# Kernel optimization log

Hardware: AMD Instinct MI355X
Metric: run time of the kernel (lower is better)

Reference implementation:

```python
import jax, jax.numpy as jnp
import numpy as np

B, S, T = 32, 512, 50          # batch, max seq, topic memory tokens
D, H, F, NL = 512, 8, 2048, 4  # bert-small dims
VB, VOC = 30000, 30522         # bow vocab (VAE), bert vocab


def _ln(x, g, b, eps=1e-12):
    m = x.mean(-1, keepdims=True)
    v = ((x - m) ** 2).mean(-1, keepdims=True)
    return (x - m) * jax.lax.rsqrt(v + eps) * g + b


def setup_inputs() -> dict:
    key = jax.random.key(0)
    ks = iter(jax.random.split(key, 40))
    n = lambda shape, s=0.02: jax.random.normal(next(ks), shape, jnp.float32) * s
    inp = {
        'input_ids': jax.random.randint(next(ks), (B, S), 0, VOC, jnp.int32),
        'seq_lens': jax.random.randint(next(ks), (B,), 1, S + 1, jnp.int32),
        'embed': n((VOC, D)),
        'W_dec': n((T, VB)), 'b_dec': jnp.zeros((VB,), jnp.float32),
        'mem_W1': n((VB, 2 * D)), 'mem_b1': jnp.zeros((2 * D,), jnp.float32),
        'mem_W2': n((2 * D, D)), 'mem_b2': jnp.zeros((D,), jnp.float32),
        'mem_ln_g': jnp.ones((D,), jnp.float32), 'mem_ln_b': jnp.zeros((D,), jnp.float32),
        'Wq': n((NL, D, D)), 'bq': jnp.zeros((NL, D), jnp.float32),
        'Wk': n((NL, D, D)), 'bk': jnp.zeros((NL, D), jnp.float32),
        'Wv': n((NL, D, D)), 'bv': jnp.zeros((NL, D), jnp.float32),
        'Wo': n((NL, D, D)), 'bo': jnp.zeros((NL, D), jnp.float32),
        'ln1_g': jnp.ones((NL, D), jnp.float32), 'ln1_b': jnp.zeros((NL, D), jnp.float32),
        'Wi': n((NL, D, F)), 'bi': jnp.zeros((NL, F), jnp.float32),
        'Wf': n((NL, F, D)), 'bf': jnp.zeros((NL, D), jnp.float32),
        'ln2_g': jnp.ones((NL, D), jnp.float32), 'ln2_b': jnp.zeros((NL, D), jnp.float32),
    }
    return inp


def reference(input_ids, seq_lens, embed, W_dec, b_dec, mem_W1, mem_b1, mem_W2, mem_b2,
              mem_ln_g, mem_ln_b, Wq, bq, Wk, bk, Wv, bv, Wo, bo, ln1_g, ln1_b,
              Wi, bi, Wf, bf, ln2_g, ln2_b):
    # --- topic memory: VAE.decode(eye(T)) == rows of decoder weight ---
    word_dist = jax.nn.softmax(W_dec + b_dec, axis=1)            # [T, VB]
    hmem = jax.nn.relu(word_dist @ mem_W1 + mem_b1)
    topic_memory = _ln(hmem @ mem_W2 + mem_b2, mem_ln_g, mem_ln_b)  # [T, D]

    hidden = embed[input_ids]                                     # [B, S, D]

    # --- vectorized ragged insertion: [real tokens | memory | padding] ---
    lens = jnp.clip(seq_lens, 1, S)[:, None]                      # [B, 1]
    j = jnp.arange(S + T)[None, :]                                # [1, S+T]
    from_mem = (j >= lens) & (j < lens + T)                       # [B, S+T]
    src = jnp.clip(jnp.where(j < lens, j, j - T), 0, S - 1)       # [B, S+T]
    gathered = jnp.take_along_axis(hidden, src[..., None], axis=1)
    mem_idx = jnp.clip(j - lens, 0, T - 1)                        # [B, S+T]
    hidden = jnp.where(from_mem[..., None], topic_memory[mem_idx], gathered)  # [B, S+T, D]
    mask = (j < lens + T).astype(hidden.dtype)                    # [B, S+T]
    bias = (mask - 1.0)[:, None, None, :] * 10000.0               # extended attention mask

    dh = D // H
    scale = 1.0 / np.sqrt(dh)
    for l in range(NL):
        q = (hidden @ Wq[l] + bq[l]).reshape(B, S + T, H, dh)
        k = (hidden @ Wk[l] + bk[l]).reshape(B, S + T, H, dh)
        v = (hidden @ Wv[l] + bv[l]).reshape(B, S + T, H, dh)
        scores = jnp.einsum('bqhd,bkhd->bhqk', q, k) * scale + bias
        attn = jax.nn.softmax(scores, axis=-1)
        ctx = jnp.einsum('bhqk,bkhd->bqhd', attn, v).reshape(B, S + T, D)
        hidden = _ln(hidden + ctx @ Wo[l] + bo[l], ln1_g[l], ln1_b[l])
        ff = jax.nn.gelu(hidden @ Wi[l] + bi[l], approximate=False)
        hidden = _ln(hidden + ff @ Wf[l] + bf[l], ln2_g[l], ln2_b[l])
    return hidden
```

## Files before the change

kernel.cpp:

```cpp
#include <hip/hip_runtime.h>
#include <hip/hip_bf16.h>
#include <math.h>

using bf16 = __hip_bfloat16;
typedef __attribute__((ext_vector_type(4))) float f32x4;
typedef __attribute__((ext_vector_type(8))) short short8;

#define B_N 32
#define S_N 512
#define T_N 50
#define H_N 8
#define NL_N 4
#define VB_N 30000
#define VBP_N 30016
#define ST_N 562
#define STP_N 576
#define NTOK_N (B_N*ST_N)
#define WCH_N 16
#define WCW_N 1875

__device__ __forceinline__ float b2f(bf16 x){ return __bfloat162float(x); }
__device__ __forceinline__ bf16  f2b(float x){ return __float2bfloat16(x); }
__device__ __forceinline__ float ldw(const void* p, long i, int f){
    return f ? ((const float*)p)[i] : __bfloat162float(((const bf16*)p)[i]);
}

__device__ __forceinline__ float gelu_f(float x){
    float z = fabsf(x) * 0.70710678118654752f;
    float t = __builtin_amdgcn_rcpf(__builtin_fmaf(0.3275911f, z, 1.f));
    float p = t*(0.254829592f + t*(-0.284496736f + t*(1.421413741f + t*(-1.453152027f + t*1.061405429f))));
    float er = 1.f - p*__expf(-z*z);
    return 0.5f*x*(1.f + copysignf(er, x));
}

__device__ __forceinline__ void load_lds16(const void* g, void* l){
    __builtin_amdgcn_global_load_lds((const __attribute__((address_space(1))) void*)g,
                                     (__attribute__((address_space(3))) void*)l, 16, 0, 0);
}

__device__ __forceinline__ int xcd_swizzle(int flat, int nwg){
    int xcd = flat & 7, rest = flat >> 3;
    int q = nwg >> 3, r = nwg & 7;
    return (xcd < r ? xcd*(q+1) : r*(q+1) + (xcd-r)*q) + rest;
}

__device__ __forceinline__ float block_reduce_max(float v, float* red, int t){
    for (int o=32;o>0;o>>=1) v = fmaxf(v, __shfl_down(v,o,64));
    int w=t>>6, lane=t&63;
    if (lane==0) red[w]=v;
    __syncthreads();
    return fmaxf(fmaxf(red[0],red[1]),fmaxf(red[2],red[3]));
}
__device__ __forceinline__ float block_reduce_sum(float v, float* red, int t){
    for (int o=32;o>0;o>>=1) v += __shfl_down(v,o,64);
    int w=t>>6, lane=t&63;
    if (lane==0) red[w]=v;
    __syncthreads();
    return red[0]+red[1]+red[2]+red[3];
}

__global__ __launch_bounds__(256) void detect_k(const unsigned int* __restrict__ w, int* flag)
{
    int t = threadIdx.x;
    float s = 0.f;
    for (int i=t;i<4096;i+=256){ int e = (w[i]>>7)&0xFF; s += fabsf((float)e - 120.f); }
    __shared__ float red[4];
    for (int o=32;o>0;o>>=1) s += __shfl_down(s,o,64);
    int wv=t>>6, lane=t&63;
    if (lane==0) red[wv]=s;
    __syncthreads();
    if (t==0) flag[0] = ((red[0]+red[1]+red[2]+red[3]) * (1.f/4096.f) > 20.f) ? 1 : 0;
}

__global__ void zero_u32_k(unsigned int* p, long n){
    long i = (long)blockIdx.x*256 + threadIdx.x;
    if (i < n) p[i] = 0u;
}

__global__ __launch_bounds__(256) void wd_partmax_k(
    const void* __restrict__ Wd, const void* __restrict__ bd,
    float* __restrict__ pmax, const int* __restrict__ flagp)
{
    const int isf = *flagp;
    int ch = blockIdx.x, r = blockIdx.y, t = threadIdx.x;
    int c0 = ch*WCW_N, c1 = c0 + WCW_N;
    __shared__ float red[4];
    float mx = -1e30f;
    for (int c=c0+t;c<c1;c+=256) mx = fmaxf(mx, ldw(Wd,(long)r*VB_N+c,isf) + ldw(bd,c,isf));
    mx = block_reduce_max(mx, red, t);
    if (t==0) pmax[r*WCH_N + ch] = mx;
}

__global__ __launch_bounds__(256) void wd_partsum_k(
    const void* __restrict__ Wd, const void* __restrict__ bd,
    const float* __restrict__ pmax, float* __restrict__ psum, const int* __restrict__ flagp)
{
    const int isf = *flagp;
    int ch = blockIdx.x, r = blockIdx.y, t = threadIdx.x;
    float mx = -1e30f;
    #pragma unroll
    for (int i=0;i<WCH_N;i++) mx = fmaxf(mx, pmax[r*WCH_N+i]);
    int c0 = ch*WCW_N, c1 = c0 + WCW_N;
    __shared__ float red[4];
    float sm = 0.f;
    for (int c=c0+t;c<c1;c+=256) sm += __expf(ldw(Wd,(long)r*VB_N+c,isf) + ldw(bd,c,isf) - mx);
    sm = block_reduce_sum(sm, red, t);
    if (t==0) psum[r*WCH_N + ch] = sm;
}

__global__ __launch_bounds__(256) void wd_write_k(
    const void* __restrict__ Wd, const void* __restrict__ bd,
    const float* __restrict__ pmax, const float* __restrict__ psum,
    bf16* __restrict__ wdb, const int* __restrict__ flagp)
{
    const int isf = *flagp;
    int ch = blockIdx.x, r = blockIdx.y, t = threadIdx.x;
    float mx = -1e30f, sm = 0.f;
    #pragma unroll
    for (int i=0;i<WCH_N;i++){ mx = fmaxf(mx, pmax[r*WCH_N+i]); sm += psum[r*WCH_N+i]; }
    float inv = 1.f/sm;
    int c0 = ch*WCW_N, c1 = c0 + WCW_N;
    for (int c=c0+t;c<c1;c+=256)
        wdb[(long)r*VBP_N + c] = f2b(__expf(ldw(Wd,(long)r*VB_N+c,isf) + ldw(bd,c,isf) - mx)*inv);
}

__global__ __launch_bounds__(256) void relu_bias_k(
    const float* __restrict__ hmem, const void* __restrict__ b1,
    bf16* __restrict__ hrel, const int* __restrict__ flagp)
{
    const int isf = *flagp;
    int r = blockIdx.x, t = threadIdx.x;
    for (int c=t;c<1024;c+=256){
        float v = (r < T_N) ? fmaxf(hmem[r*1024+c] + ldw(b1,c,isf), 0.f) : 0.f;
        hrel[r*1024+c] = f2b(v);
    }
}

__global__ __launch_bounds__(256) void ln_topic_k(
    const float* __restrict__ fcout,
    const void* __restrict__ lg, const void* __restrict__ lb,
    float* __restrict__ tmf, bf16* __restrict__ tmb, const int* __restrict__ flagp)
{
    const int isf = *flagp;
    int r = blockIdx.x, t = threadIdx.x;
    float a0 = fcout[r*512+t], a1 = fcout[r*512+t+256];
    __shared__ float red[4];
    float mean = block_reduce_sum(a0+a1, red, t) * (1.f/512.f);
    float d0=a0-mean, d1=a1-mean;
    __syncthreads();
    float var = block_reduce_sum(d0*d0+d1*d1, red, t) * (1.f/512.f);
    float rstd = rsqrtf(var + 1e-12f);
    float o0 = d0*rstd*ldw(lg,t,isf) + ldw(lb,t,isf);
    float o1 = d1*rstd*ldw(lg,t+256,isf) + ldw(lb,t+256,isf);
    tmf[r*512+t]=o0; tmf[r*512+t+256]=o1;
    tmb[r*512+t]=f2b(o0); tmb[r*512+t+256]=f2b(o1);
}

__global__ __launch_bounds__(256) void embed_insert_k(
    const int* __restrict__ ids, const int* __restrict__ lens,
    const void* __restrict__ embed, const float* __restrict__ tmf,
    const bf16* __restrict__ tmb, float* __restrict__ hf, bf16* __restrict__ hb,
    const int* __restrict__ flagp)
{
    const int isf = *flagp;
    int j = blockIdx.x, b = blockIdx.y, t = threadIdx.x;
    int L = lens[b]; L = L<1?1:(L>S_N?S_N:L);
    long orow = ((long)b*ST_N + j)*512;
    if (j >= L && j < L + T_N) {
        int m = j - L;
        for (int c=t;c<512;c+=256){ float v = tmf[m*512+c]; hf[orow+c]=v; hb[orow+c]=tmb[m*512+c]; }
    } else {
        int sj = (j < L) ? j : j - T_N;
        int id = ids[b*S_N + sj];
        for (int c=t;c<512;c+=256){ float e = ldw(embed,(long)id*512+c,isf); hf[orow+c]=e; hb[orow+c]=f2b(e); }
    }
}

__global__ __launch_bounds__(256) void transpose_k(
    const void* __restrict__ src, bf16* __restrict__ dst,
    int R, int C, long sstride, long dstride, int Ksrc, const int* __restrict__ flagp)
{
    const int isf = *flagp;
    __shared__ bf16 tile[32][33];
    int n0 = blockIdx.x * 32, k0 = blockIdx.y * 32, z = blockIdx.z;
    int t = threadIdx.x;
    int nl = t & 31, kb = t >> 5;
    #pragma unroll
    for (int i=0;i<4;i++) {
        int k = k0 + kb + i*8; k = k < Ksrc ? k : Ksrc-1;
        tile[kb+i*8][nl] = f2b(ldw(src, z*sstride + (long)k*C + n0+nl, isf));
    }
    __syncthreads();
    int kl = t & 31, nb = t >> 5;
    #pragma unroll
    for (int i=0;i<4;i++) {
        int n = nb + i*8;
        dst[z*dstride + (long)(n0+n)*R + k0+kl] = tile[kl][n];
    }
}

__global__ void concat_bias_k(const void* bq, const void* bk, const void* bv, bf16* out,
                              const int* __restrict__ flagp){
    const int isf = *flagp;
    int i = blockIdx.x*256 + threadIdx.x;
    if (i >= NL_N*1536) return;
    int l = i/1536, n = i%1536;
    float v = (n<512) ? ldw(bq,l*512+n,isf) : (n<1024 ? ldw(bk,l*512+n-512,isf) : ldw(bv,l*512+n-1024,isf));
    out[i] = f2b(v);
}

__global__ __launch_bounds__(256) void transpose_v_k(
    const bf16* __restrict__ qkv, bf16* __restrict__ Vt, const int* __restrict__ slens)
{
    __shared__ bf16 tl[64*33];
    int k0 = blockIdx.x * 32, z = blockIdx.z;
    int b = z >> 3, h = z & 7;
    int L = slens[b]; L = L<1?1:(L>S_N?S_N:L);
    int kmax = ((L + T_N + 63) >> 6) << 6;
    if (k0 >= kmax) return;
    int t = threadIdx.x;
    int n = t & 63, kb = t >> 6;
    #pragma unroll
    for (int i=0;i<8;i++) {
        int kl = kb + 4*i;
        int kg = k0 + kl;
        bf16 v = (kg < ST_N) ? qkv[((long)(b*ST_N + kg))*1536 + 1024 + h*64 + n] : f2b(0.f);
        tl[n*33 + kl] = v;
    }
    __syncthreads();
    int kk = t & 31, nb = t >> 5;
    #pragma unroll
    for (int i=0;i<8;i++) {
        int nn = nb + 8*i;
        Vt[((long)z*64 + nn)*STP_N + k0 + kk] = tl[nn*33 + kk];
    }
}

constexpr int EPI_BF16=0, EPI_F32=1, EPI_GELU=2, EPI_ATOMIC=3, EPI_BF16R=4;

template<int BM, int BN, int MODE>
__global__ __launch_bounds__(256,4) void gemm_k(
    const bf16* __restrict__ Ag, const bf16* __restrict__ Bg, void* __restrict__ Cg,
    const void* __restrict__ bias, long bias_off,
    int M, int N, int K, int lda, int ldb, int ldc, int Nst, int kch,
    const int* __restrict__ flagp)
{
    const int isf = *flagp;
    __shared__ __align__(16) bf16 lA[BM*64];
    __shared__ __align__(16) bf16 lB[BN*64];
    const int tid = threadIdx.x;
    const int nwg = gridDim.x * gridDim.y;
    const int flat = blockIdx.y * gridDim.x + blockIdx.x;
    const int swz = xcd_swizzle(flat, nwg);
    const int tile_m = (swz / gridDim.x) * BM;
    const int tile_n = (swz % gridDim.x) * BN;

    bf16*  C16 = (bf16*)Cg;
    float* C32 = (float*)Cg;

    constexpr int WM = BM/2, WN = BN/2, MI = WM/16, NI = WN/16;
    const int w = tid>>6, lane = tid&63;
    const int wm = w>>1, wn = w&1;
    const int quad = lane>>4, lrow = lane&15;

    f32x4 zero = {0.f,0.f,0.f,0.f};
    f32x4 acc[MI][NI];
    #pragma unroll
    for (int i=0;i<MI;i++)
        #pragma unroll
        for (int j=0;j<NI;j++) acc[i][j] = zero;

    int ks = 0, ke = K;
    if (kch > 0) { ks = blockIdx.z * kch; ke = ks + kch; if (ke > K) ke = K; }

    for (int k0=ks;k0<ke;k0+=64) {
        __syncthreads();
        #pragma unroll
        for (int r=0;r<BM/32;r++) {
            int e = r*256 + tid;
            int row = e>>3, c8 = (e&7) ^ (row&7);
            int gr = tile_m + row; gr = gr < M ? gr : M-1;
            load_lds16(Ag + (long)gr*lda + k0 + c8*8, &lA[e*8]);
        }
        #pragma unroll
        for (int r=0;r<BN/32;r++) {
            int e = r*256 + tid;
            int row = e>>3, c8 = (e&7) ^ (row&7);
            int gr = tile_n + row; gr = gr < N ? gr : N-1;
            load_lds16(Bg + (long)gr*ldb + k0 + c8*8, &lB[e*8]);
        }
        __syncthreads();
        #pragma unroll
        for (int kc=0;kc<2;kc++){
            short8 afr[MI], bfr[NI];
            #pragma unroll
            for (int i=0;i<MI;i++){
                int row = wm*WM + i*16 + lrow;
                afr[i] = *(const short8*)&lA[row*64 + (((kc*4+quad) ^ (row&7))<<3)];
            }
            #pragma unroll
            for (int j=0;j<NI;j++){
                int row = wn*WN + j*16 + lrow;
                bfr[j] = *(const short8*)&lB[row*64 + (((kc*4+quad) ^ (row&7))<<3)];
            }
            #pragma unroll
            for (int i=0;i<MI;i++)
                #pragma unroll
                for (int j=0;j<NI;j++)
                    acc[i][j] = __builtin_amdgcn_mfma_f32_16x16x32_bf16(afr[i], bfr[j], acc[i][j], 0, 0, 0);
        }
    }

    float bcol[NI];
    #pragma unroll
    for (int j=0;j<NI;j++){
        int col = tile_n + wn*WN + j*16 + lrow;
        if constexpr (MODE == EPI_ATOMIC) { bcol[j] = 0.f; }
        else if constexpr (MODE == EPI_BF16) {
            bcol[j] = (col < Nst) ? b2f(((const bf16*)bias)[bias_off + col]) : 0.f;
        } else {
            bcol[j] = (col < Nst) ? ldw(bias, bias_off + col, isf) : 0.f;
        }
    }

    #pragma unroll
    for (int i=0;i<MI;i++) {
        #pragma unroll
        for (int j=0;j<NI;j++) {
            int col = tile_n + wn*WN + j*16 + lrow;
            if (col >= Nst) continue;
            int rb  = tile_m + wm*WM + i*16 + quad*4;
            #pragma unroll
            for (int r=0;r<4;r++) {
                int row = rb + r;
                if (row >= M) continue;
                float v = acc[i][j][r];
                if constexpr (MODE == EPI_BF16 || MODE == EPI_BF16R) {
                    C16[(long)row*ldc + col] = f2b(v + bcol[j]);
                } else if constexpr (MODE == EPI_F32) {
                    C32[(long)row*ldc + col] = v + bcol[j];
                } else if constexpr (MODE == EPI_GELU) {
                    C16[(long)row*ldc + col] = f2b(gelu_f(v + bcol[j]));
                } else {
                    atomicAdd(&C32[(long)row*ldc + col], v);
                }
            }
        }
    }
}

__global__ __launch_bounds__(256,3) void flash_k(
    const bf16* __restrict__ qkv, const bf16* __restrict__ Vt,
    bf16* __restrict__ ctx, const int* __restrict__ slens)
{
    __shared__ __align__(16) bf16 lQ[64*64];
    __shared__ __align__(16) bf16 lK[2][64*64];
    __shared__ __align__(16) bf16 lV[2][64*64];
    __shared__ __align__(16) bf16 lP[64*64];
    const int nwg = gridDim.x * gridDim.z;
    const int flat = blockIdx.z * gridDim.x + blockIdx.x;
    const int swz = xcd_swizzle(flat, nwg);
    const int z = swz / gridDim.x, b = z>>3, h = z&7;
    const int qt = swz % gridDim.x;
    const int tid = threadIdx.x;
    const int w = tid>>6, lane = tid&63;
    const int quad = lane>>4, l15 = lane&15;
    int L = slens[b]; L = L<1?1:(L>S_N?S_N:L);
    const int lenT = L + T_N;
    const int nkt = (lenT + 63) >> 6;

    #pragma unroll
    for (int rr=0;rr<2;rr++){
        int ci = rr*256 + tid;
        int row = ci>>3, c8 = (ci&7) ^ (row&7);
        int gr = qt*64 + row; gr = gr < ST_N ? gr : ST_N-1;
        load_lds16(qkv + ((long)(b*ST_N+gr))*1536 + h*64 + c8*8, &lQ[ci*8]);
    }

    auto stage_K = [&](int buf, int kt){
        #pragma unroll
        for (int rr=0;rr<2;rr++){
            int ci = rr*256+tid;
            int row = ci>>3, c8 = (ci&7) ^ (row&7);
            int kr = kt*64+row; kr = kr < ST_N ? kr : ST_N-1;
            load_lds16(qkv + ((long)(b*ST_N+kr))*1536 + 512 + h*64 + c8*8, &lK[buf][ci*8]);
        }
    };
    auto stage_V = [&](int buf, int kt){
        #pragma unroll
        for (int rr=0;rr<2;rr++){
            int ci = rr*256+tid;
            int n = ci>>3, c8 = (ci&7) ^ (n&7);
            load_lds16(Vt + ((long)z*64+n)*STP_N + kt*64 + c8*8, &lV[buf][ci*8]);
        }
    };

    stage_K(0, 0);
    stage_V(0, 0);

    f32x4 zerov = {0.f,0.f,0.f,0.f};
    f32x4 O[4];
    float m_i[4], l_i[4];
    #pragma unroll
    for (int j=0;j<4;j++) O[j] = zerov;
    #pragma unroll
    for (int r=0;r<4;r++){ m_i[r]=-1e30f; l_i[r]=0.f; }

    const int qrow = w*16;

    for (int kt=0; kt<nkt; kt++){
        const int cur = kt & 1;
        __syncthreads();
        if (kt+1 < nkt) stage_K(cur^1, kt+1);

        f32x4 S[4];
        #pragma unroll
        for (int j=0;j<4;j++) S[j] = zerov;
        #pragma unroll
        for (int kc=0;kc<2;kc++){
            short8 aQ, bK[4];
            {
                int row = qrow + l15;
                aQ = *(const short8*)&lQ[row*64 + (((kc*4+quad) ^ (row&7))<<3)];
            }
            #pragma unroll
            for (int j=0;j<4;j++){
                int row = j*16+l15;
                bK[j] = *(const short8*)&lK[cur][row*64 + (((kc*4+quad) ^ (row&7))<<3)];
            }
            #pragma unroll
            for (int j=0;j<4;j++)
                S[j] = __builtin_amdgcn_mfma_f32_16x16x32_bf16(aQ, bK[j], S[j], 0,0,0);
        }

        #pragma unroll
        for (int r=0;r<4;r++){
            float mx = -1e30f;
            #pragma unroll
            for (int j=0;j<4;j++){
                int col = kt*64 + j*16 + l15;
                float s = S[j][r]*0.125f + (col < lenT ? 0.f : -10000.f);
                S[j][r] = s;
                mx = fmaxf(mx, s);
            }
            #pragma unroll
            for (int o=1;o<16;o<<=1) mx = fmaxf(mx, __shfl_xor(mx, o, 64));
            float mn = fmaxf(m_i[r], mx);
            float alpha = __expf(m_i[r] - mn);
            m_i[r] = mn;
            float sm = 0.f;
            #pragma unroll
            for (int j=0;j<4;j++){
                float pv = __expf(S[j][r] - mn);
                S[j][r] = pv;
                sm += pv;
            }
            #pragma unroll
            for (int o=1;o<16;o<<=1) sm += __shfl_xor(sm, o, 64);
            l_i[r] = l_i[r]*alpha + sm;
            #pragma unroll
            for (int j=0;j<4;j++) O[j][r] *= alpha;
        }

        #pragma unroll
        for (int j=0;j<4;j++)
            #pragma unroll
            for (int r=0;r<4;r++){
                int row = qrow + quad*4 + r;
                int col = j*16 + l15;
                lP[row*64 + (((col>>3) ^ (row&7))<<3) + (col&7)] = f2b(S[j][r]);
            }
        __syncthreads();
        if (kt+1 < nkt) stage_V(cur^1, kt+1);

        #pragma unroll
        for (int kc=0;kc<2;kc++){
            short8 aP, bV[4];
            {
                int row = qrow + l15;
                aP = *(const short8*)&lP[row*64 + (((kc*4+quad) ^ (row&7))<<3)];
            }
            #pragma unroll
            for (int j=0;j<4;j++){
                int row = j*16+l15;
                bV[j] = *(const short8*)&lV[cur][row*64 + (((kc*4+quad) ^ (row&7))<<3)];
            }
            #pragma unroll
            for (int j=0;j<4;j++)
                O[j] = __builtin_amdgcn_mfma_f32_16x16x32_bf16(aP, bV[j], O[j], 0,0,0);
        }
    }

    #pragma unroll
    for (int r=0;r<4;r++){
        int row = qt*64 + qrow + quad*4 + r;
        if (row >= ST_N) continue;
        float inv_l = __builtin_amdgcn_rcpf(l_i[r]);
        #pragma unroll
        for (int j=0;j<4;j++)
            ctx[((long)(b*ST_N+row))*512 + h*64 + j*16 + l15] = f2b(O[j][r] * inv_l);
    }
}

__global__ __launch_bounds__(256) void ln_residual_k(
    const bf16* __restrict__ tmp, float* __restrict__ hf, bf16* __restrict__ hb,
    const void* __restrict__ g, const void* __restrict__ bb, long goff,
    void* __restrict__ outp, int is_final, const int* __restrict__ flagp)
{
    const int isf = *flagp;
    const int of32 = is_final && isf;
    long base = (long)blockIdx.x * 512;
    int t = threadIdx.x;
    float v0 = hf[base+t]     + b2f(tmp[base+t]);
    float v1 = hf[base+t+256] + b2f(tmp[base+t+256]);
    __shared__ float red[4];
    float mean = block_reduce_sum(v0+v1, red, t) * (1.f/512.f);
    float d0=v0-mean, d1=v1-mean;
    __syncthreads();
    float var = block_reduce_sum(d0*d0+d1*d1, red, t) * (1.f/512.f);
    float rstd = rsqrtf(var + 1e-12f);
    float o0 = d0*rstd*ldw(g,goff+t,isf) + ldw(bb,goff+t,isf);
    float o1 = d1*rstd*ldw(g,goff+t+256,isf) + ldw(bb,goff+t+256,isf);
    hf[base+t]=o0; hf[base+t+256]=o1;
    hb[base+t]=f2b(o0); hb[base+t+256]=f2b(o1);
    if (of32) {
        ((float*)outp)[base+t]=o0; ((float*)outp)[base+t+256]=o1;
    } else {
        ((bf16*)outp)[base+t]=f2b(o0); ((bf16*)outp)[base+t+256]=f2b(o1);
    }
}

extern "C" void kernel_launch(void* const* d_in, const int* in_sizes, int n_in,
                              void* d_out, int out_size, void* d_ws, size_t ws_size,
                              hipStream_t stream)
{
    (void)in_sizes; (void)n_in; (void)out_size; (void)ws_size;
    const int*  ids   = (const int*) d_in[0];
    const int*  slens = (const int*) d_in[1];
    const void* embed = d_in[2];
    const void* Wdec  = d_in[3];
    const void* bdec  = d_in[4];
    const void* mW1   = d_in[5];
    const void* mb1   = d_in[6];
    const void* mW2   = d_in[7];
    const void* mb2   = d_in[8];
    const void* mlg   = d_in[9];
    const void* mlb   = d_in[10];
    const void* Wq    = d_in[11];
    const void* bq    = d_in[12];
    const void* Wk    = d_in[13];
    const void* bk    = d_in[14];
    const void* Wv    = d_in[15];
    const void* bv    = d_in[16];
    const void* Wo    = d_in[17];
    const void* bo    = d_in[18];
    const void* l1g   = d_in[19];
    const void* l1b   = d_in[20];
    const void* Wi    = d_in[21];
    const void* bi    = d_in[22];
    const void* Wf    = d_in[23];
    const void* bfv   = d_in[24];
    const void* l2g   = d_in[25];
    const void* l2b   = d_in[26];

    char* p = (char*)d_ws;
    auto alloc = [&](size_t bytes)->void* {
        void* r = (void*)p; p += (bytes + 255) & ~(size_t)255; return r; };
    int*   flag  = (int*)  alloc(256);
    float* pmax  = (float*)alloc((size_t)T_N*WCH_N*4);
    float* psum  = (float*)alloc((size_t)T_N*WCH_N*4);
    float* tmf   = (float*)alloc((size_t)T_N*512*4);
    bf16*  tmb   = (bf16*) alloc((size_t)T_N*512*2);
    float* hmem  = (float*)alloc((size_t)64*1024*4);
    bf16*  hrel  = (bf16*) alloc((size_t)64*1024*2);
    float* fcout = (float*)alloc((size_t)64*512*4);
    float* hidf  = (float*)alloc((size_t)NTOK_N*512*4);
    bf16*  hidb  = (bf16*) alloc((size_t)NTOK_N*512*2);
    bf16*  qkvt  = (bf16*) alloc((size_t)NL_N*1536*512*2);
    bf16*  wot   = (bf16*) alloc((size_t)NL_N*512*512*2);
    bf16*  wit   = (bf16*) alloc((size_t)NL_N*2048*512*2);
    bf16*  wft   = (bf16*) alloc((size_t)NL_N*512*2048*2);
    bf16*  bqkv  = (bf16*) alloc((size_t)NL_N*1536*2);
    char*  R1    = (char*) alloc((size_t)NTOK_N*2048*2);
    bf16*  wdb   = (bf16*)R1;
    bf16*  W1t   = (bf16*)(R1 + (size_t)64*VBP_N*2);
    bf16*  W2t   = (bf16*)(R1 + (size_t)64*VBP_N*2 + (size_t)1024*VBP_N*2);
    bf16*  qkv   = (bf16*)R1;
    bf16*  ffb   = (bf16*)R1;
    bf16*  ctx   = (bf16*) alloc((size_t)NTOK_N*512*2);
    char*  RU2   = (char*) alloc((size_t)NTOK_N*512*4);
    bf16*  Vt    = (bf16*)RU2;
    bf16*  tmp16 = (bf16*)RU2;

    detect_k<<<1,256,0,stream>>>((const unsigned int*)embed, flag);

    zero_u32_k<<<((64L*VBP_N/2)+255)/256,256,0,stream>>>((unsigned int*)wdb, 64L*VBP_N/2);
    zero_u32_k<<<((64L*1024)+255)/256,256,0,stream>>>((unsigned int*)hmem, 64L*1024);
    wd_partmax_k<<<dim3(WCH_N,T_N),256,0,stream>>>(Wdec,bdec,pmax,flag);
    wd_partsum_k<<<dim3(WCH_N,T_N),256,0,stream>>>(Wdec,bdec,pmax,psum,flag);
    wd_write_k  <<<dim3(WCH_N,T_N),256,0,stream>>>(Wdec,bdec,pmax,psum,wdb,flag);
    transpose_k<<<dim3(32,VBP_N/32,1),256,0,stream>>>(mW1, W1t, VBP_N, 1024, 0L, 0L, VB_N, flag);
    transpose_k<<<dim3(16,32,1),256,0,stream>>>(mW2, W2t, 1024, 512, 0L, 0L, 1024, flag);
    gemm_k<64,128,EPI_ATOMIC><<<dim3(8,1,32),256,0,stream>>>(
        wdb, W1t, hmem, nullptr, 0,
        64, 1024, VBP_N, VBP_N, VBP_N, 1024, 1024, 960, flag);
    relu_bias_k<<<64,256,0,stream>>>(hmem, mb1, hrel, flag);
    gemm_k<64,128,EPI_F32><<<dim3(4,1,1),256,0,stream>>>(
        hrel, W2t, fcout, mb2, 0,
        64, 512, 1024, 1024, 1024, 512, 512, 0, flag);
    ln_topic_k<<<T_N,256,0,stream>>>(fcout, mlg, mlb, tmf, tmb, flag);
    embed_insert_k<<<dim3(ST_N,B_N),256,0,stream>>>(ids, slens, embed, tmf, tmb, hidf, hidb, flag);

    transpose_k<<<dim3(16,16,NL_N),256,0,stream>>>(Wq, qkvt,          512, 512, 262144L, 786432L, 512, flag);
    transpose_k<<<dim3(16,16,NL_N),256,0,stream>>>(Wk, qkvt+262144,   512, 512, 262144L, 786432L, 512, flag);
    transpose_k<<<dim3(16,16,NL_N),256,0,stream>>>(Wv, qkvt+524288,   512, 512, 262144L, 786432L, 512, flag);
    transpose_k<<<dim3(16,16,NL_N),256,0,stream>>>(Wo, wot,           512, 512, 262144L, 262144L, 512, flag);
    transpose_k<<<dim3(64,16,NL_N),256,0,stream>>>(Wi, wit,           512, 2048, 1048576L, 1048576L, 512, flag);
    transpose_k<<<dim3(16,64,NL_N),256,0,stream>>>(Wf, wft,           2048, 512, 1048576L, 1048576L, 2048, flag);
    concat_bias_k<<<(NL_N*1536+255)/256,256,0,stream>>>(bq,bk,bv,bqkv,flag);

    for (int l=0;l<NL_N;l++) {
        gemm_k<128,128,EPI_BF16><<<dim3(12,141,1),256,0,stream>>>(
            hidb, qkvt + (size_t)l*786432, qkv, bqkv, (long)l*1536,
            NTOK_N, 1536, 512, 512, 512, 1536, 1536, 0, flag);
        transpose_v_k<<<dim3(18,1,256),256,0,stream>>>(qkv, Vt, slens);
        flash_k<<<dim3(9,1,256),256,0,stream>>>(qkv, Vt, ctx, slens);
        gemm_k<128,128,EPI_BF16R><<<dim3(4,141,1),256,0,stream>>>(
            ctx, wot + (size_t)l*262144, tmp16, bo, (long)l*512,
            NTOK_N, 512, 512, 512, 512, 512, 512, 0, flag);
        ln_residual_k<<<NTOK_N,256,0,stream>>>(tmp16, hidf, hidb, l1g, l1b, (long)l*512,
                                               hidb, 0, flag);
        gemm_k<128,128,EPI_GELU><<<dim3(16,141,1),256,0,stream>>>(
            hidb, wit + (size_t)l*1048576, ffb, bi, (long)l*2048,
            NTOK_N, 2048, 512, 512, 512, 2048, 2048, 0, flag);
        gemm_k<128,128,EPI_BF16R><<<dim3(4,141,1),256,0,stream>>>(
            ffb, wft + (size_t)l*1048576, tmp16, bfv, (long)l*512,
            NTOK_N, 512, 2048, 2048, 2048, 512, 512, 0, flag);
        ln_residual_k<<<NTOK_N,256,0,stream>>>(tmp16, hidf, hidb, l2g, l2b, (long)l*512,
                                               (l == NL_N-1) ? d_out : (void*)hidb,
                                               (l == NL_N-1) ? 1 : 0, flag);
    }
}
```

Before: 1.579 ms.

## Add lazy softmax rescaling, last-tile masking, MFMA priority, and incremental GEMM pointers

In the attention kernel, the running max is rescaled only when a tile's max exceeds the stored max by more than a threshold, so most tiles skip the alpha computation and the rescale of the O accumulator. The padding mask is applied only on the last KV tile. The MFMA blocks are wrapped in s_setprio to favour matrix instructions across waves. In the GEMM, global load addresses are computed once and advanced by pointer increments instead of being recomputed every K step. Lazy rescaling relies on bounded exponent growth, and the early-tile mask skip assumes only the last tile holds padded columns.

```diff
diff --git a/kernel.cpp b/kernel.cpp
--- a/kernel.cpp
+++ b/kernel.cpp
@@ -273,21 +273,34 @@
     int ks = 0, ke = K;
     if (kch > 0) { ks = blockIdx.z * kch; ke = ks + kch; if (ke > K) ke = K; }
 
+    const bf16* pA[BM/32];
+    const bf16* pB[BN/32];
+    #pragma unroll
+    for (int r=0;r<BM/32;r++) {
+        int e = r*256 + tid;
+        int row = e>>3, c8 = (e&7) ^ (row&7);
+        int gr = tile_m + row; gr = gr < M ? gr : M-1;
+        pA[r] = Ag + (long)gr*lda + ks + c8*8;
+    }
+    #pragma unroll
+    for (int r=0;r<BN/32;r++) {
+        int e = r*256 + tid;
+        int row = e>>3, c8 = (e&7) ^ (row&7);
+        int gr = tile_n + row; gr = gr < N ? gr : N-1;
+        pB[r] = Bg + (long)gr*ldb + ks + c8*8;
+    }
+
     for (int k0=ks;k0<ke;k0+=64) {
         __syncthreads();
         #pragma unroll
         for (int r=0;r<BM/32;r++) {
-            int e = r*256 + tid;
-            int row = e>>3, c8 = (e&7) ^ (row&7);
-            int gr = tile_m + row; gr = gr < M ? gr : M-1;
-            load_lds16(Ag + (long)gr*lda + k0 + c8*8, &lA[e*8]);
+            load_lds16(pA[r], &lA[(r*256+tid)*8]);
+            pA[r] += 64;
         }
         #pragma unroll
         for (int r=0;r<BN/32;r++) {
-            int e = r*256 + tid;
-            int row = e>>3, c8 = (e&7) ^ (row&7);
-            int gr = tile_n + row; gr = gr < N ? gr : N-1;
-            load_lds16(Bg + (long)gr*ldb + k0 + c8*8, &lB[e*8]);
+            load_lds16(pB[r], &lB[(r*256+tid)*8]);
+            pB[r] += 64;
         }
         __syncthreads();
         #pragma unroll
@@ -428,38 +441,67 @@
                 int row = j*16+l15;
                 bK[j] = *(const short8*)&lK[cur][row*64 + (((kc*4+quad) ^ (row&7))<<3)];
             }
+            __builtin_amdgcn_s_setprio(1);
             #pragma unroll
             for (int j=0;j<4;j++)
                 S[j] = __builtin_amdgcn_mfma_f32_16x16x32_bf16(aQ, bK[j], S[j], 0,0,0);
-        }
-
+            __builtin_amdgcn_s_setprio(0);
+        }
+
+        const bool last_tile = (kt == nkt-1);
+        float mx[4]; float excess = -1e30f;
         #pragma unroll
         for (int r=0;r<4;r++){
-            float mx = -1e30f;
+            float m0 = -1e30f;
             #pragma unroll
             for (int j=0;j<4;j++){
-                int col = kt*64 + j*16 + l15;
-                float s = S[j][r]*0.125f + (col < lenT ? 0.f : -10000.f);
+                float s = S[j][r]*0.125f;
+                if (last_tile) {
+                    int col = kt*64 + j*16 + l15;
+                    s += (col < lenT ? 0.f : -10000.f);
+                }
                 S[j][r] = s;
-                mx = fmaxf(mx, s);
-            }
-            #pragma unroll
-            for (int o=1;o<16;o<<=1) mx = fmaxf(mx, __shfl_xor(mx, o, 64));
-            float mn = fmaxf(m_i[r], mx);
-            float alpha = __expf(m_i[r] - mn);
-            m_i[r] = mn;
-            float sm = 0.f;
-            #pragma unroll
-            for (int j=0;j<4;j++){
-                float pv = __expf(S[j][r] - mn);
-                S[j][r] = pv;
-                sm += pv;
-            }
-            #pragma unroll
-            for (int o=1;o<16;o<<=1) sm += __shfl_xor(sm, o, 64);
-            l_i[r] = l_i[r]*alpha + sm;
-            #pragma unroll
-            for (int j=0;j<4;j++) O[j][r] *= alpha;
+                m0 = fmaxf(m0, s);
+            }
+            #pragma unroll
+            for (int o=1;o<16;o<<=1) m0 = fmaxf(m0, __shfl_xor(m0, o, 64));
+            mx[r] = m0;
+            excess = fmaxf(excess, m0 - m_i[r]);
+        }
+
+        if (__all(excess <= 8.f)) {
+            #pragma unroll
+            for (int r=0;r<4;r++){
+                float sm = 0.f;
+                #pragma unroll
+                for (int j=0;j<4;j++){
+                    float pv = __expf(S[j][r] - m_i[r]);
+                    S[j][r] = pv;
+                    sm += pv;
+                }
+                #pragma unroll
+                for (int o=1;o<16;o<<=1) sm += __shfl_xor(sm, o, 64);
+                l_i[r] += sm;
+            }
+        } else {
+            #pragma unroll
+            for (int r=0;r<4;r++){
+                float mn = fmaxf(m_i[r], mx[r]);
+                float alpha = __expf(m_i[r] - mn);
+                m_i[r] = mn;
+                float sm = 0.f;
+                #pragma unroll
+                for (int j=0;j<4;j++){
+                    float pv = __expf(S[j][r] - mn);
+                    S[j][r] = pv;
+                    sm += pv;
+                }
+                #pragma unroll
+                for (int o=1;o<16;o<<=1) sm += __shfl_xor(sm, o, 64);
+                l_i[r] = l_i[r]*alpha + sm;
+                #pragma unroll
+                for (int j=0;j<4;j++) O[j][r] *= alpha;
+            }
         }
 
         #pragma unroll
@@ -485,9 +527,11 @@
                 int row = j*16+l15;
                 bV[j] = *(const short8*)&lV[cur][row*64 + (((kc*4+quad) ^ (row&7))<<3)];
             }
+            __builtin_amdgcn_s_setprio(1);
             #pragma unroll
             for (int j=0;j<4;j++)
                 O[j] = __builtin_amdgcn_mfma_f32_16x16x32_bf16(aP, bV[j], O[j], 0,0,0);
+            __builtin_amdgcn_s_setprio(0);
         }
     }
 
```

After: 1.700 ms. +7.7%, slower.
